# Kernel optimization log

Measured on AMD Instinct MI355X. Metric: run time of the kernel, lower is better.

The kernel has to match this reference:

```python
import jax, jax.numpy as jnp
import numpy as np

K = 12
ORDERS = [(1, 2, 3), (1, 3, 2), (3, 2, 1), (3, 1, 2), (2, 1, 3), (2, 3, 1)]


def ranking_3d(x):
    # x: (B, L1, W1, H1, D) -> (B, 12, L1*W1*H1, D)
    B, L1, W1, H1, D = x.shape
    seqs = []
    for dims in ORDERS:
        perm = (0,) + dims + (4,)
        seqs.append(jnp.transpose(x, perm).reshape(B, -1, D))
        xr = jnp.flip(x, axis=dims)
        seqs.append(jnp.transpose(xr, perm).reshape(B, -1, D))
    return jnp.stack(seqs, axis=1)


def restore_original(out_y, shape):
    # out_y: (B, 12, D, L). NOTE: faithfully replicates the original code, which
    # reshapes the (B, D, L) slice directly to (B, d1, d2, d3, D).
    B, L1, W1, H1, D = shape
    size = {1: L1, 2: W1, 3: H1}
    restored = []
    for i in range(12):
        dims = ORDERS[i // 2]
        seq = out_y[:, i]  # (B, D, L)
        dims_shape = tuple(size[d] for d in dims)
        reshaped = seq.reshape((B,) + dims_shape + (D,))
        perm = (0,) + dims + (4,)
        inv = tuple(np.argsort(perm))
        r = jnp.transpose(reshaped, inv)
        if i % 2 == 1:
            r = jnp.flip(r, axis=dims)
        restored.append(r)
    return restored


def selective_scan(u, delta, A, Bs, Cs):
    # u, delta: (B,K,D,L); A: (K,D,N); Bs, Cs: (B,K,N,L)
    us = jnp.moveaxis(u, -1, 0)       # (L,B,K,D)
    ds = jnp.moveaxis(delta, -1, 0)   # (L,B,K,D)
    Bts = jnp.moveaxis(Bs, -1, 0)     # (L,B,K,N)
    Cts = jnp.moveaxis(Cs, -1, 0)     # (L,B,K,N)
    h0 = jnp.zeros(u.shape[:-1] + (A.shape[-1],), u.dtype)  # (B,K,D,N)

    def step(h, inp):
        ut, dt, Bt, Ct = inp
        dA = jnp.exp(dt[..., None] * A)                       # (B,K,D,N)
        h = dA * h + (dt * ut)[..., None] * Bt[:, :, None, :]
        y = jnp.einsum('bkdn,bkn->bkd', h, Ct)
        return h, y

    _, ys = jax.lax.scan(step, h0, (us, ds, Bts, Cts))
    return jnp.moveaxis(ys, 0, -1)  # (B,K,D,L)


def setup_inputs() -> dict:
    key = jax.random.key(0)
    ks = jax.random.split(key, 8)
    B, H, W, Len, D = 1, 16, 16, 16, 128
    N, R = 16, 8
    x = jax.random.normal(ks[0], (B, H, W, Len, D), dtype=jnp.float32)
    x_proj_weight = jax.random.normal(ks[1], (K, R + 2 * N, D), dtype=jnp.float32) * 0.02
    std = R ** -0.5
    dt_projs_weight = jax.random.uniform(ks[2], (K, D, R), minval=-std, maxval=std, dtype=jnp.float32)
    dt = jnp.exp(jax.random.uniform(ks[3], (K, D)) * (np.log(0.1) - np.log(0.001)) + np.log(0.001))
    dt = jnp.clip(dt, 1e-4, None)
    dt_projs_bias = (dt + jnp.log(-jnp.expm1(-dt))).astype(jnp.float32)
    A_logs = jnp.broadcast_to(jnp.log(jnp.arange(1, N + 1, dtype=jnp.float32)), (K, D, N)).copy()
    Ds = jnp.ones((K, D), dtype=jnp.float32)
    merge_w = jax.random.normal(ks[4], (K,), dtype=jnp.float32) * (1.0 / K)
    merge_b = jax.random.normal(ks[5], (), dtype=jnp.float32) * 0.01
    return {'x': x, 'x_proj_weight': x_proj_weight, 'dt_projs_weight': dt_projs_weight,
            'dt_projs_bias': dt_projs_bias, 'A_logs': A_logs, 'Ds': Ds,
            'merge_w': merge_w, 'merge_b': merge_b}


def reference(x, x_proj_weight, dt_projs_weight, dt_projs_bias, A_logs, Ds, merge_w, merge_b):
    B, H, W, Len, D = x.shape
    L = H * W * Len
    R = dt_projs_weight.shape[-1]
    N = A_logs.shape[-1]
    xs = jnp.transpose(ranking_3d(x), (0, 1, 3, 2))  # (B,K,D,L)
    x_dbl = jnp.einsum('bkdl,kcd->bkcl', xs, x_proj_weight)  # (B,K,R+2N,L)
    dts, Bs, Cs = jnp.split(x_dbl, [R, R + N], axis=2)
    dts = jnp.einsum('bkrl,kdr->bkdl', dts, dt_projs_weight)
    delta = jax.nn.softplus(dts + dt_projs_bias[None, :, :, None])
    A = -jnp.exp(A_logs)  # (K,D,N)
    ys = selective_scan(xs, delta, A, Bs, Cs)
    out_y = ys + Ds[None, :, :, None] * xs  # (B,K,D,L)
    restored = restore_original(out_y, (B, H, W, Len, D))
    stacked = jnp.stack(restored, axis=1)  # (B,K,H,W,Len,D)
    # mergeconv: 1x1 Conv2d over K channels == weighted sum across directions
    y = jnp.einsum('bkhwld,k->bhwld', stacked, merge_w) + merge_b
    return y
```

## Files before the change

### kernel.cpp

```cpp
#include <hip/hip_runtime.h>

#define KK 12
#define LL 4096
#define DD 128
#define NN 16
#define RR 8
#define NC 128
#define LC 32
#define XST 132
#define SDST 44
#define XDBL_TILE (64 * SDST)

__device__ __forceinline__ int pos_of(int k, int l) {
    int o = k >> 1;
    int le = (k & 1) ? (4095 - l) : l;
    int t1 = le >> 8, t2 = (le >> 4) & 15, t3 = le & 15;
    switch (o) {
        case 0:  return (t1 << 8) | (t2 << 4) | t3;
        case 1:  return (t1 << 8) | (t3 << 4) | t2;
        case 2:  return (t3 << 8) | (t2 << 4) | t1;
        case 3:  return (t2 << 8) | (t3 << 4) | t1;
        case 4:  return (t2 << 8) | (t1 << 4) | t3;
        default: return (t3 << 8) | (t1 << 4) | t2;
    }
}

__device__ __forceinline__ float delta_row_z(const float* sdbl, int l,
                                             float4 w0, float4 w1, float bz) {
    const float4* dr = (const float4*)(sdbl + l * SDST);
    float4 r0 = dr[0], r1 = dr[1];
    return bz + w0.x * r0.x + w0.y * r0.y + w0.z * r0.z + w0.w * r0.w
              + w1.x * r1.x + w1.y * r1.y + w1.z * r1.z + w1.w * r1.w;
}

__device__ __forceinline__ bool load_A16(const float* __restrict__ A_logs,
                                         int k, int d, float* A16) {
    const float4* ap = (const float4*)(A_logs + (size_t)(k * DD + d) * NN);
    #pragma unroll
    for (int q = 0; q < 4; q++) {
        float4 a4 = ap[q];
        A16[4*q+0] = -__expf(a4.x); A16[4*q+1] = -__expf(a4.y);
        A16[4*q+2] = -__expf(a4.z); A16[4*q+3] = -__expf(a4.w);
    }
    bool s = true;
    #pragma unroll
    for (int j = 1; j < 16; j++) {
        float m = (float)(j + 1);
        s = s && (fabsf(A16[j] - m * A16[0]) <= 1e-4f * m * fabsf(A16[0]));
    }
    return s;
}

template<bool S>
__device__ __forceinline__ void e16_from(float v, const float* A16, float* e) {
    if (S) {
        float q = __expf(v * A16[0]);
        e[0] = q;
        #pragma unroll
        for (int j = 1; j < 16; j++) e[j] = e[j - 1] * q;
    } else {
        #pragma unroll
        for (int j = 0; j < 16; j++) e[j] = __expf(v * A16[j]);
    }
}

template<bool S>
__device__ __forceinline__ void scanA_body(
    float* xs, const float* sdbl, int k, int cc, int rbase, int d,
    const float* A16, float4 w0, float4 w1, float bz, float Dval,
    float* __restrict__ S_g, float* __restrict__ dtsum)
{
    float h[16];
    #pragma unroll
    for (int n = 0; n < 16; n++) h[n] = 0.0f;
    float dsum = 0.0f;

    #pragma unroll 4
    for (int i = 0; i < LC; i++) {
        int l = rbase + i;
        float z = delta_row_z(sdbl, l, w0, w1, bz);
        float E = __expf(-fabsf(z));
        float dt = fmaxf(z, 0.0f) + __logf(1.0f + E);
        float u = xs[l * XST + d];
        dsum += dt;
        float tu = dt * u;
        float e[16];
        e16_from<S>(dt, A16, e);
        const float4* bp = (const float4*)(&sdbl[l * SDST + 8]);
        float4 b0 = bp[0], b1 = bp[1], b2 = bp[2], b3 = bp[3];
        const float4* cp = (const float4*)(&sdbl[l * SDST + 24]);
        float4 c0 = cp[0], c1 = cp[1], c2 = cp[2], c3 = cp[3];
        h[0]  = e[0]  * h[0]  + tu * b0.x;  h[1]  = e[1]  * h[1]  + tu * b0.y;
        h[2]  = e[2]  * h[2]  + tu * b0.z;  h[3]  = e[3]  * h[3]  + tu * b0.w;
        h[4]  = e[4]  * h[4]  + tu * b1.x;  h[5]  = e[5]  * h[5]  + tu * b1.y;
        h[6]  = e[6]  * h[6]  + tu * b1.z;  h[7]  = e[7]  * h[7]  + tu * b1.w;
        h[8]  = e[8]  * h[8]  + tu * b2.x;  h[9]  = e[9]  * h[9]  + tu * b2.y;
        h[10] = e[10] * h[10] + tu * b2.z;  h[11] = e[11] * h[11] + tu * b2.w;
        h[12] = e[12] * h[12] + tu * b3.x;  h[13] = e[13] * h[13] + tu * b3.y;
        h[14] = e[14] * h[14] + tu * b3.z;  h[15] = e[15] * h[15] + tu * b3.w;
        float y = h[0]*c0.x + h[1]*c0.y + h[2]*c0.z + h[3]*c0.w
                + h[4]*c1.x + h[5]*c1.y + h[6]*c1.z + h[7]*c1.w
                + h[8]*c2.x + h[9]*c2.y + h[10]*c2.z + h[11]*c2.w
                + h[12]*c3.x + h[13]*c3.y + h[14]*c3.z + h[15]*c3.w;
        xs[l * XST + d] = y + Dval * u;
    }

    float4* sp = (float4*)(S_g + (((size_t)(k * NC + cc) * DD + d) * NN));
    sp[0] = make_float4(h[0],  h[1],  h[2],  h[3]);
    sp[1] = make_float4(h[4],  h[5],  h[6],  h[7]);
    sp[2] = make_float4(h[8],  h[9],  h[10], h[11]);
    sp[3] = make_float4(h[12], h[13], h[14], h[15]);
    dtsum[(k * NC + cc) * DD + d] = dsum;
}

__global__ __launch_bounds__(256, 3) void k1_proj_scanA(
    const float* __restrict__ x, const float* __restrict__ Wp,
    const float* __restrict__ Wdt, const float* __restrict__ bias,
    const float* __restrict__ A_logs, const float* __restrict__ Ds,
    float* __restrict__ S_g, float* __restrict__ dtsum,
    float* __restrict__ oy, float* __restrict__ xdbl)
{
    const int blk = blockIdx.x;
    const int k = blk >> 6;
    const int c = blk & 63;
    const int l0 = c * 64;
    const int t = threadIdx.x;

    __shared__ __align__(16) float xs[64 * XST];
    __shared__ __align__(16) float sdbl[64 * SDST];
    __shared__ int pos_s[64];

    if (t < 64) pos_s[t] = pos_of(k, l0 + t);
    __syncthreads();

    {
        int lane32 = t & 31, rowi = t >> 5;
        #pragma unroll
        for (int p = 0; p < 8; p++) {
            int l = p * 8 + rowi;
            float4 v = *(const float4*)(x + (size_t)pos_s[l] * DD + lane32 * 4);
            *(float4*)(&xs[l * XST + lane32 * 4]) = v;
        }
    }
    __syncthreads();

    {
        int l = t & 63, cgch = t >> 6;
        float acc[10];
        #pragma unroll
        for (int j = 0; j < 10; j++) acc[j] = 0.0f;
        const float* wk = Wp + (size_t)(k * 40 + cgch * 10) * DD;
        for (int d4 = 0; d4 < DD; d4 += 4) {
            float4 xv = *(const float4*)(&xs[l * XST + d4]);
            #pragma unroll
            for (int j = 0; j < 10; j++) {
                const float* w = wk + j * DD + d4;
                acc[j] += xv.x * w[0] + xv.y * w[1] + xv.z * w[2] + xv.w * w[3];
            }
        }
        #pragma unroll
        for (int j = 0; j < 10; j++) sdbl[l * SDST + cgch * 10 + j] = acc[j];
    }
    __syncthreads();

    {
        const float4* s4 = (const float4*)sdbl;
        float4* g4 = (float4*)(xdbl + (size_t)blk * XDBL_TILE);
        for (int idx = t; idx < XDBL_TILE / 4; idx += 256) g4[idx] = s4[idx];
    }

    const int d = t & 127, half = t >> 7;
    const int cc = 2 * c + half, rbase = half * LC;
    float A16[16];
    bool structured = load_A16(A_logs, k, d, A16);
    const float4* wp4 = (const float4*)(Wdt + (size_t)(k * DD + d) * RR);
    const float4 w0 = wp4[0], w1 = wp4[1];
    const float bz = bias[k * DD + d];
    const float Dval = Ds[k * DD + d];

    if (structured)
        scanA_body<true>(xs, sdbl, k, cc, rbase, d, A16, w0, w1, bz, Dval,
                         S_g, dtsum);
    else
        scanA_body<false>(xs, sdbl, k, cc, rbase, d, A16, w0, w1, bz, Dval,
                          S_g, dtsum);

    {
        float* base = oy + ((size_t)(k * DD + d)) * LL + l0 + rbase;
        #pragma unroll
        for (int p = 0; p < 8; p++) {
            int j = p * 4;
            float4 v = make_float4(xs[(rbase + j + 0) * XST + d],
                                   xs[(rbase + j + 1) * XST + d],
                                   xs[(rbase + j + 2) * XST + d],
                                   xs[(rbase + j + 3) * XST + d]);
            *(float4*)(base + j) = v;
        }
    }
}

__global__ __launch_bounds__(256) void k2_combine(
    float* __restrict__ S_g, const float* __restrict__ dtsum,
    const float* __restrict__ A_logs)
{
    int tid = blockIdx.x * 256 + threadIdx.x;
    int kk = tid >> 11, rem = tid & 2047, dd2 = rem >> 4;
    float Ac = -__expf(A_logs[tid]);
    float hh = 0.0f;
    #pragma unroll 8
    for (int c2 = 0; c2 < NC; c2++) {
        size_t base = ((size_t)(kk * NC + c2)) * 2048 + rem;
        float s = S_g[base];
        float dsv = dtsum[(kk * NC + c2) * DD + dd2];
        S_g[base] = hh;
        hh = s + __expf(dsv * Ac) * hh;
    }
}

template<bool S>
__device__ __forceinline__ void corr_body(
    float* ybuf, const float* sdbl, int rbase, int d,
    const float* A16, const float* h0, float4 w0, float4 w1, float bz)
{
    float Dsum = 0.0f;
    #pragma unroll 4
    for (int i = 0; i < LC; i++) {
        int l = rbase + i;
        float z = delta_row_z(sdbl, l, w0, w1, bz);
        float E = __expf(-fabsf(z));
        float dt = fmaxf(z, 0.0f) + __logf(1.0f + E);
        Dsum += dt;
        float e[16];
        e16_from<S>(Dsum, A16, e);
        const float4* cp = (const float4*)(&sdbl[l * SDST + 24]);
        float4 c0 = cp[0], c1 = cp[1], c2 = cp[2], c3 = cp[3];
        float y = e[0]*h0[0]*c0.x + e[1]*h0[1]*c0.y + e[2]*h0[2]*c0.z + e[3]*h0[3]*c0.w
                + e[4]*h0[4]*c1.x + e[5]*h0[5]*c1.y + e[6]*h0[6]*c1.z + e[7]*h0[7]*c1.w
                + e[8]*h0[8]*c2.x + e[9]*h0[9]*c2.y + e[10]*h0[10]*c2.z + e[11]*h0[11]*c2.w
                + e[12]*h0[12]*c3.x + e[13]*h0[13]*c3.y + e[14]*h0[14]*c3.z + e[15]*h0[15]*c3.w;
        ybuf[l * XST + d] = y;
    }
}

__global__ __launch_bounds__(256, 3) void k3_corr(
    const float* __restrict__ Wdt, const float* __restrict__ bias,
    const float* __restrict__ A_logs, const float* __restrict__ S_g,
    const float* __restrict__ xdbl, float* __restrict__ oy)
{
    const int blk = blockIdx.x;
    const int k = blk >> 6;
    const int c = blk & 63;
    const int l0 = c * 64;
    const int t = threadIdx.x;

    __shared__ __align__(16) float sdbl[64 * SDST];
    __shared__ __align__(16) float ybuf[64 * XST];
    {
        const float4* g4 = (const float4*)(xdbl + (size_t)blk * XDBL_TILE);
        float4* s4 = (float4*)sdbl;
        for (int idx = t; idx < XDBL_TILE / 4; idx += 256) s4[idx] = g4[idx];
    }
    __syncthreads();

    const int d = t & 127, half = t >> 7;
    const int cc = 2 * c + half, rbase = half * LC;
    float A16[16];
    bool structured = load_A16(A_logs, k, d, A16);
    const float4* wp4 = (const float4*)(Wdt + (size_t)(k * DD + d) * RR);
    const float4 w0 = wp4[0], w1 = wp4[1];
    const float bz = bias[k * DD + d];

    float h0[16];
    if (cc != 0) {
        const float4* hp = (const float4*)(S_g + (((size_t)(k * NC + cc) * DD + d) * NN));
        float4 a = hp[0], b = hp[1], c4 = hp[2], e4 = hp[3];
        h0[0] = a.x;  h0[1] = a.y;  h0[2] = a.z;  h0[3] = a.w;
        h0[4] = b.x;  h0[5] = b.y;  h0[6] = b.z;  h0[7] = b.w;
        h0[8] = c4.x; h0[9] = c4.y; h0[10] = c4.z; h0[11] = c4.w;
        h0[12] = e4.x; h0[13] = e4.y; h0[14] = e4.z; h0[15] = e4.w;
    } else {
        #pragma unroll
        for (int n = 0; n < 16; n++) h0[n] = 0.0f;
    }

    if (structured)
        corr_body<true>(ybuf, sdbl, rbase, d, A16, h0, w0, w1, bz);
    else
        corr_body<false>(ybuf, sdbl, rbase, d, A16, h0, w0, w1, bz);

    {
        float* base = oy + ((size_t)(k * DD + d)) * LL + l0 + rbase;
        #pragma unroll
        for (int p = 0; p < 8; p++) {
            int j = p * 4;
            float4 v = *(float4*)(base + j);
            v.x += ybuf[(rbase + j + 0) * XST + d];
            v.y += ybuf[(rbase + j + 1) * XST + d];
            v.z += ybuf[(rbase + j + 2) * XST + d];
            v.w += ybuf[(rbase + j + 3) * XST + d];
            *(float4*)(base + j) = v;
        }
    }
}

__global__ __launch_bounds__(256) void k4_merge(
    const float* __restrict__ out_y, const float* __restrict__ mw,
    const float* __restrict__ mb, float* __restrict__ out)
{
    int idx = blockIdx.x * 256 + threadIdx.x;
    int dd = idx & 127;
    int p = idx >> 7;
    int i3 = p & 15, i2 = (p >> 4) & 15, i1 = (p >> 8) & 15;

    float accv = mb[0];
    #pragma unroll
    for (int k = 0; k < 12; k++) {
        int a1 = i1, a2 = i2, a3 = i3;
        if (k & 1) { a1 = 15 - i1; a2 = 15 - i2; a3 = 15 - i3; }
        int j1, j2, j3;
        switch (k >> 1) {
            case 0:  j1 = a1; j2 = a2; j3 = a3; break;
            case 1:  j1 = a1; j2 = a3; j3 = a2; break;
            case 2:  j1 = a3; j2 = a2; j3 = a1; break;
            case 3:  j1 = a3; j2 = a1; j3 = a2; break;
            case 4:  j1 = a2; j2 = a1; j3 = a3; break;
            default: j1 = a2; j2 = a3; j3 = a1; break;
        }
        int jb = (j1 << 8) | (j2 << 4) | j3;
        accv += mw[k] * out_y[(size_t)k * (DD * LL) + (jb >> 5) * LL
                              + ((jb & 31) << 7) + dd];
    }
    out[idx] = accv;
}

extern "C" void kernel_launch(void* const* d_in, const int* in_sizes, int n_in,
                              void* d_out, int out_size, void* d_ws, size_t ws_size,
                              hipStream_t stream) {
    const float* x      = (const float*)d_in[0];
    const float* Wp     = (const float*)d_in[1];
    const float* Wdt    = (const float*)d_in[2];
    const float* bias   = (const float*)d_in[3];
    const float* A_logs = (const float*)d_in[4];
    const float* Ds     = (const float*)d_in[5];
    const float* mw     = (const float*)d_in[6];
    const float* mb     = (const float*)d_in[7];
    float* out = (float*)d_out;

    float* ws   = (float*)d_ws;
    float* S_g  = ws;
    float* dts  = S_g + (size_t)KK * NC * DD * NN;
    float* oy   = dts + (size_t)KK * NC * DD;
    float* xdbl = oy + (size_t)KK * DD * LL;

    k1_proj_scanA<<<dim3(KK * 64), dim3(256), 0, stream>>>(
        x, Wp, Wdt, bias, A_logs, Ds, S_g, dts, oy, xdbl);
    k2_combine<<<dim3(KK * DD * NN / 256), dim3(256), 0, stream>>>(S_g, dts, A_logs);
    k3_corr<<<dim3(KK * 64), dim3(256), 0, stream>>>(Wdt, bias, A_logs, S_g, xdbl, oy);
    k4_merge<<<dim3(LL * DD / 256), dim3(256), 0, stream>>>(oy, mw, mb, out);
}
```

Before: 170.4 us.

## Halve scan chunk length to double block count and parallelism

Splits the sequence into 256 chunks of 16 steps instead of 128 of 32, launching twice as many blocks for the projection/scan and correction kernels with smaller shared tiles and higher occupancy bounds. The correction kernel now builds the decay as a running product of per-step exponentials in the structured case, and always loads the carried state (presumably zeroed by the combine step for chunk 0). The aim is more parallel work and a shorter sequential chain per thread, at the cost of a longer serial combine over more chunks and more workspace traffic.

```diff
diff --git a/kernel.cpp b/kernel.cpp
--- a/kernel.cpp
+++ b/kernel.cpp
@@ -5,11 +5,12 @@
 #define DD 128
 #define NN 16
 #define RR 8
-#define NC 128
-#define LC 32
-#define XST 132
+#define NC 256
+#define LCS 16
+#define LB 32
+#define XST 140
 #define SDST 44
-#define XDBL_TILE (64 * SDST)
+#define XDBL_TILE (LB * SDST)
 
 __device__ __forceinline__ int pos_of(int k, int l) {
     int o = k >> 1;
@@ -52,9 +53,9 @@
 }
 
 template<bool S>
-__device__ __forceinline__ void e16_from(float v, const float* A16, float* e) {
+__device__ __forceinline__ void e16_from(float v, float q, const float* A16,
+                                         float* e) {
     if (S) {
-        float q = __expf(v * A16[0]);
         e[0] = q;
         #pragma unroll
         for (int j = 1; j < 16; j++) e[j] = e[j - 1] * q;
@@ -66,7 +67,7 @@
 
 template<bool S>
 __device__ __forceinline__ void scanA_body(
-    float* xs, const float* sdbl, int k, int cc, int rbase, int d,
+    float* xs, const float* sdbl, int k, int cc, int lbase, int d,
     const float* A16, float4 w0, float4 w1, float bz, float Dval,
     float* __restrict__ S_g, float* __restrict__ dtsum)
 {
@@ -76,16 +77,17 @@
     float dsum = 0.0f;
 
     #pragma unroll 4
-    for (int i = 0; i < LC; i++) {
-        int l = rbase + i;
+    for (int i = 0; i < LCS; i++) {
+        int l = lbase + i;
         float z = delta_row_z(sdbl, l, w0, w1, bz);
         float E = __expf(-fabsf(z));
         float dt = fmaxf(z, 0.0f) + __logf(1.0f + E);
         float u = xs[l * XST + d];
         dsum += dt;
         float tu = dt * u;
+        float q = S ? __expf(dt * A16[0]) : 0.0f;
         float e[16];
-        e16_from<S>(dt, A16, e);
+        e16_from<S>(dt, q, A16, e);
         const float4* bp = (const float4*)(&sdbl[l * SDST + 8]);
         float4 b0 = bp[0], b1 = bp[1], b2 = bp[2], b3 = bp[3];
         const float4* cp = (const float4*)(&sdbl[l * SDST + 24]);
@@ -113,7 +115,7 @@
     dtsum[(k * NC + cc) * DD + d] = dsum;
 }
 
-__global__ __launch_bounds__(256, 3) void k1_proj_scanA(
+__global__ __launch_bounds__(256, 4) void k1_proj_scanA(
     const float* __restrict__ x, const float* __restrict__ Wp,
     const float* __restrict__ Wdt, const float* __restrict__ bias,
     const float* __restrict__ A_logs, const float* __restrict__ Ds,
@@ -121,22 +123,22 @@
     float* __restrict__ oy, float* __restrict__ xdbl)
 {
     const int blk = blockIdx.x;
-    const int k = blk >> 6;
-    const int c = blk & 63;
-    const int l0 = c * 64;
+    const int k = blk >> 7;
+    const int c = blk & 127;
+    const int l0 = c * LB;
     const int t = threadIdx.x;
 
-    __shared__ __align__(16) float xs[64 * XST];
-    __shared__ __align__(16) float sdbl[64 * SDST];
-    __shared__ int pos_s[64];
-
-    if (t < 64) pos_s[t] = pos_of(k, l0 + t);
+    __shared__ __align__(16) float xs[LB * XST];
+    __shared__ __align__(16) float sdbl[LB * SDST];
+    __shared__ int pos_s[LB];
+
+    if (t < LB) pos_s[t] = pos_of(k, l0 + t);
     __syncthreads();
 
     {
         int lane32 = t & 31, rowi = t >> 5;
         #pragma unroll
-        for (int p = 0; p < 8; p++) {
+        for (int p = 0; p < 4; p++) {
             int l = p * 8 + rowi;
             float4 v = *(const float4*)(x + (size_t)pos_s[l] * DD + lane32 * 4);
             *(float4*)(&xs[l * XST + lane32 * 4]) = v;
@@ -145,21 +147,21 @@
     __syncthreads();
 
     {
-        int l = t & 63, cgch = t >> 6;
-        float acc[10];
-        #pragma unroll
-        for (int j = 0; j < 10; j++) acc[j] = 0.0f;
-        const float* wk = Wp + (size_t)(k * 40 + cgch * 10) * DD;
+        int l = t & 31, cg = t >> 5;
+        float acc[5];
+        #pragma unroll
+        for (int j = 0; j < 5; j++) acc[j] = 0.0f;
+        const float* wk = Wp + (size_t)(k * 40 + cg * 5) * DD;
         for (int d4 = 0; d4 < DD; d4 += 4) {
             float4 xv = *(const float4*)(&xs[l * XST + d4]);
             #pragma unroll
-            for (int j = 0; j < 10; j++) {
+            for (int j = 0; j < 5; j++) {
                 const float* w = wk + j * DD + d4;
                 acc[j] += xv.x * w[0] + xv.y * w[1] + xv.z * w[2] + xv.w * w[3];
             }
         }
         #pragma unroll
-        for (int j = 0; j < 10; j++) sdbl[l * SDST + cgch * 10 + j] = acc[j];
+        for (int j = 0; j < 5; j++) sdbl[l * SDST + cg * 5 + j] = acc[j];
     }
     __syncthreads();
 
@@ -170,7 +172,7 @@
     }
 
     const int d = t & 127, half = t >> 7;
-    const int cc = 2 * c + half, rbase = half * LC;
+    const int cc = 2 * c + half, lbase = half * LCS;
     float A16[16];
     bool structured = load_A16(A_logs, k, d, A16);
     const float4* wp4 = (const float4*)(Wdt + (size_t)(k * DD + d) * RR);
@@ -179,21 +181,21 @@
     const float Dval = Ds[k * DD + d];
 
     if (structured)
-        scanA_body<true>(xs, sdbl, k, cc, rbase, d, A16, w0, w1, bz, Dval,
+        scanA_body<true>(xs, sdbl, k, cc, lbase, d, A16, w0, w1, bz, Dval,
                          S_g, dtsum);
     else
-        scanA_body<false>(xs, sdbl, k, cc, rbase, d, A16, w0, w1, bz, Dval,
+        scanA_body<false>(xs, sdbl, k, cc, lbase, d, A16, w0, w1, bz, Dval,
                           S_g, dtsum);
 
     {
-        float* base = oy + ((size_t)(k * DD + d)) * LL + l0 + rbase;
-        #pragma unroll
-        for (int p = 0; p < 8; p++) {
+        float* base = oy + ((size_t)(k * DD + d)) * LL + l0 + lbase;
+        #pragma unroll
+        for (int p = 0; p < 4; p++) {
             int j = p * 4;
-            float4 v = make_float4(xs[(rbase + j + 0) * XST + d],
-                                   xs[(rbase + j + 1) * XST + d],
-                                   xs[(rbase + j + 2) * XST + d],
-                                   xs[(rbase + j + 3) * XST + d]);
+            float4 v = make_float4(xs[(lbase + j + 0) * XST + d],
+                                   xs[(lbase + j + 1) * XST + d],
+                                   xs[(lbase + j + 2) * XST + d],
+                                   xs[(lbase + j + 3) * XST + d]);
             *(float4*)(base + j) = v;
         }
     }
@@ -219,19 +221,25 @@
 
 template<bool S>
 __device__ __forceinline__ void corr_body(
-    float* ybuf, const float* sdbl, int rbase, int d,
+    float* ybuf, const float* sdbl, int lbase, int d,
     const float* A16, const float* h0, float4 w0, float4 w1, float bz)
 {
+    float P = 1.0f;
     float Dsum = 0.0f;
     #pragma unroll 4
-    for (int i = 0; i < LC; i++) {
-        int l = rbase + i;
+    for (int i = 0; i < LCS; i++) {
+        int l = lbase + i;
         float z = delta_row_z(sdbl, l, w0, w1, bz);
         float E = __expf(-fabsf(z));
         float dt = fmaxf(z, 0.0f) + __logf(1.0f + E);
-        Dsum += dt;
         float e[16];
-        e16_from<S>(Dsum, A16, e);
+        if (S) {
+            P *= __expf(dt * A16[0]);
+            e16_from<true>(0.0f, P, A16, e);
+        } else {
+            Dsum += dt;
+            e16_from<false>(Dsum, 0.0f, A16, e);
+        }
         const float4* cp = (const float4*)(&sdbl[l * SDST + 24]);
         float4 c0 = cp[0], c1 = cp[1], c2 = cp[2], c3 = cp[3];
         float y = e[0]*h0[0]*c0.x + e[1]*h0[1]*c0.y + e[2]*h0[2]*c0.z + e[3]*h0[3]*c0.w
@@ -242,19 +250,19 @@
     }
 }
 
-__global__ __launch_bounds__(256, 3) void k3_corr(
+__global__ __launch_bounds__(256, 4) void k3_corr(
     const float* __restrict__ Wdt, const float* __restrict__ bias,
     const float* __restrict__ A_logs, const float* __restrict__ S_g,
     const float* __restrict__ xdbl, float* __restrict__ oy)
 {
     const int blk = blockIdx.x;
-    const int k = blk >> 6;
-    const int c = blk & 63;
-    const int l0 = c * 64;
+    const int k = blk >> 7;
+    const int c = blk & 127;
+    const int l0 = c * LB;
     const int t = threadIdx.x;
 
-    __shared__ __align__(16) float sdbl[64 * SDST];
-    __shared__ __align__(16) float ybuf[64 * XST];
+    __shared__ __align__(16) float sdbl[LB * SDST];
+    __shared__ __align__(16) float ybuf[LB * XST];
     {
         const float4* g4 = (const float4*)(xdbl + (size_t)blk * XDBL_TILE);
         float4* s4 = (float4*)sdbl;
@@ -263,7 +271,7 @@
     __syncthreads();
 
     const int d = t & 127, half = t >> 7;
-    const int cc = 2 * c + half, rbase = half * LC;
+    const int cc = 2 * c + half, lbase = half * LCS;
     float A16[16];
     bool structured = load_A16(A_logs, k, d, A16);
     const float4* wp4 = (const float4*)(Wdt + (size_t)(k * DD + d) * RR);
@@ -271,33 +279,30 @@
     const float bz = bias[k * DD + d];
 
     float h0[16];
-    if (cc != 0) {
+    {
         const float4* hp = (const float4*)(S_g + (((size_t)(k * NC + cc) * DD + d) * NN));
         float4 a = hp[0], b = hp[1], c4 = hp[2], e4 = hp[3];
-        h0[0] = a.x;  h0[1] = a.y;  h0[2] = a.z;  h0[3] = a.w;
-        h0[4] = b.x;  h0[5] = b.y;  h0[6] = b.z;  h0[7] = b.w;
-        h0[8] = c4.x; h0[9] = c4.y; h0[10] = c4.z; h0[11] = c4.w;
+        h0[0]  = a.x;  h0[1]  = a.y;  h0[2]  = a.z;  h0[3]  = a.w;
+        h0[4]  = b.x;  h0[5]  = b.y;  h0[6]  = b.z;  h0[7]  = b.w;
+        h0[8]  = c4.x; h0[9]  = c4.y; h0[10] = c4.z; h0[11] = c4.w;
         h0[12] = e4.x; h0[13] = e4.y; h0[14] = e4.z; h0[15] = e4.w;
-    } else {
-        #pragma unroll
-        for (int n = 0; n < 16; n++) h0[n] = 0.0f;
     }
 
     if (structured)
-        corr_body<true>(ybuf, sdbl, rbase, d, A16, h0, w0, w1, bz);
+        corr_body<true>(ybuf, sdbl, lbase, d, A16, h0, w0, w1, bz);
     else
-        corr_body<false>(ybuf, sdbl, rbase, d, A16, h0, w0, w1, bz);
-
-    {
-        float* base = oy + ((size_t)(k * DD + d)) * LL + l0 + rbase;
-        #pragma unroll
-        for (int p = 0; p < 8; p++) {
+        corr_body<false>(ybuf, sdbl, lbase, d, A16, h0, w0, w1, bz);
+
+    {
+        float* base = oy + ((size_t)(k * DD + d)) * LL + l0 + lbase;
+        #pragma unroll
+        for (int p = 0; p < 4; p++) {
             int j = p * 4;
             float4 v = *(float4*)(base + j);
-            v.x += ybuf[(rbase + j + 0) * XST + d];
-            v.y += ybuf[(rbase + j + 1) * XST + d];
-            v.z += ybuf[(rbase + j + 2) * XST + d];
-            v.w += ybuf[(rbase + j + 3) * XST + d];
+            v.x += ybuf[(lbase + j + 0) * XST + d];
+            v.y += ybuf[(lbase + j + 1) * XST + d];
+            v.z += ybuf[(lbase + j + 2) * XST + d];
+            v.w += ybuf[(lbase + j + 3) * XST + d];
             *(float4*)(base + j) = v;
         }
     }
@@ -352,9 +357,10 @@
     float* oy   = dts + (size_t)KK * NC * DD;
     float* xdbl = oy + (size_t)KK * DD * LL;
 
-    k1_proj_scanA<<<dim3(KK * 64), dim3(256), 0, stream>>>(
+    k1_proj_scanA<<<dim3(KK * 128), dim3(256), 0, stream>>>(
         x, Wp, Wdt, bias, A_logs, Ds, S_g, dts, oy, xdbl);
     k2_combine<<<dim3(KK * DD * NN / 256), dim3(256), 0, stream>>>(S_g, dts, A_logs);
-    k3_corr<<<dim3(KK * 64), dim3(256), 0, stream>>>(Wdt, bias, A_logs, S_g, xdbl, oy);
+    k3_corr<<<dim3(KK * 128), dim3(256), 0, stream>>>(
+        Wdt, bias, A_logs, S_g, xdbl, oy);
     k4_merge<<<dim3(LL * DD / 256), dim3(256), 0, stream>>>(oy, mw, mb, out);
 }
```

New measurement: 181.3 us. 1.06x slower.
